# Kernel optimization log

Measured on AMD Instinct MI355X. Metric: run time of the kernel, lower is better.

Reference implementation:

```python
import jax, jax.numpy as jnp
import numpy as np

B, C, W, H = 4, 256, 64, 64

def setup_inputs() -> dict:
    key = jax.random.key(0)
    ks = jax.random.split(key, 6)
    return {
        "fm_source": jax.random.normal(ks[0], (B, C, W, H), dtype=jnp.float32),
        "fm_reference": jax.random.normal(ks[1], (B, C, W, H), dtype=jnp.float32),
        "w_lambda": jax.random.normal(ks[2], (1, C, 1, 1), dtype=jnp.float32) * 0.05,
        "b_lambda": jax.random.normal(ks[3], (1,), dtype=jnp.float32) * 0.05,
        "w_beta": jax.random.normal(ks[4], (1, C, 1, 1), dtype=jnp.float32) * 0.05,
        "b_beta": jax.random.normal(ks[5], (1,), dtype=jnp.float32) * 0.05,
    }

def reference(fm_source, fm_reference, w_lambda, b_lambda, w_beta, b_beta):
    b, c, w, h = fm_reference.shape
    n = w * h
    # 1x1 convs on the reference feature map -> per-pixel scalars, flattened to [B, N]
    wl = w_lambda.reshape(c)
    wb = w_beta.reshape(c)
    ref_flat = fm_reference.reshape(b, c, n)   # [B, C, N]
    src_flat = fm_source.reshape(b, c, n)      # [B, C, N]
    old_lambda = jnp.einsum("bcn,c->bn", ref_flat, wl) + b_lambda[0]  # [B, N]
    old_beta = jnp.einsum("bcn,c->bn", ref_flat, wb) + b_beta[0]      # [B, N]
    # energy[b, i, j] = <src pixel i, ref pixel j> over channels
    energy = jnp.einsum("bci,bcj->bij", src_flat, ref_flat)  # [B, N, N]
    attention = jax.nn.softmax(energy, axis=-1)              # softmax over ref pixels j
    # new_lambda[b, i] = sum_j old_lambda[b, j] * attention[b, i, j]
    new_lambda = jnp.einsum("bj,bij->bi", old_lambda, attention).reshape(b, 1, w, h)
    new_beta = jnp.einsum("bj,bij->bi", old_beta, attention).reshape(b, 1, w, h)
    # broadcast modulation over the 256 channels
    return new_lambda * fm_source + new_beta
```

## Files before the change

kernel.cpp:

```cpp
#include <hip/hip_runtime.h>


#define B_ 4
#define C_ 256
#define N_ 4096
#define LOG2E 1.44269504f
#define SHIFT2 86.5617f
#define JSLICE 8
#define BN_ (B_ * N_)
#define NT_ 16

typedef _Float16 half_t;
typedef _Float16 v8h  __attribute__((ext_vector_type(8)));
typedef float    v16f __attribute__((ext_vector_type(16)));

#define GLDS16(g, l) __builtin_amdgcn_global_load_lds(                         \
    (const __attribute__((address_space(1))) void*)(g),                        \
    (__attribute__((address_space(3))) void*)(l), 16, 0, 0)

#define TILE_SEC(T, ACC0, ACC1, LAM, BET, DO_FIN, FACC0, FACC1, FLAM, FBET)    \
  {                                                                            \
    __syncthreads();                                                           \
    if ((T) + 1 < NT_) {                                                       \
      const half_t* g = bBase + (size_t)((T) + 1) * 8192;                      \
      _Pragma("unroll")                                                        \
      for (int q = 0; q < 2; q++) {                                            \
        int chunk = q * 8 + wv;                                                \
        GLDS16(g + (size_t)chunk * 512 + (size_t)lane * 8,                     \
               &lds[((T) + 1) & 1][(size_t)chunk * 512]);                      \
      }                                                                        \
    }                                                                          \
    LAM = oL[(T) * 32 + l31];                                                  \
    BET = oB[(T) * 32 + l31];                                                  \
    const half_t* bt = lds[(T) & 1] + (size_t)lane * 8;                        \
    _Pragma("unroll")                                                          \
    for (int r = 0; r < 16; r++) { ACC0[r] = -SHIFT2; ACC1[r] = 0.f; }         \
    _Pragma("unroll")                                                          \
    for (int kb = 0; kb < 8; kb++) {                                           \
      ACC0 = __builtin_amdgcn_mfma_f32_32x32x16_f16(                           \
          a[kb], *(const v8h*)(bt + (size_t)kb * 512), ACC0, 0, 0, 0);         \
      ACC1 = __builtin_amdgcn_mfma_f32_32x32x16_f16(                           \
          a[kb + 8], *(const v8h*)(bt + (size_t)(kb + 8) * 512), ACC1, 0,0,0); \
      if (DO_FIN) {                                                            \
        _Pragma("unroll")                                                      \
        for (int rr = 2 * kb; rr < 2 * kb + 2; rr++) {                         \
          float p = __builtin_amdgcn_exp2f(FACC0[rr] + FACC1[rr]);             \
          sp[rr] += p; sl[rr] += p * FLAM; sb[rr] += p * FBET;                 \
        }                                                                      \
      }                                                                        \
    }                                                                          \
  }

__global__ void k_prep(const float* __restrict__ src,
                       const float* __restrict__ ref,
                       const float* __restrict__ wl,
                       const float* __restrict__ wb,
                       half_t* __restrict__ s16, half_t* __restrict__ r16,
                       float* __restrict__ oldLp, float* __restrict__ oldBp,
                       float* __restrict__ sums ) {
    __shared__ float tile[64][65];
    __shared__ float red[8][64];
    int z  = blockIdx.z;
    int isRef = z >> 2;
    int b  = z & 3;
    const float* in  = isRef ? ref : src;
    half_t*      out = isRef ? r16 : s16;
    float scale      = isRef ? 1.0f : LOG2E;
    int c0 = blockIdx.y * 64;
    int n0 = blockIdx.x * 64;
    int tid = threadIdx.x;
    if (z == 0) {
        int gid = (blockIdx.y * 64 + blockIdx.x) * 256 + tid;
        if (gid < 3 * BN_) sums[gid] = 0.f;
    }
    int tx = tid & 15, ty = tid >> 4;
#pragma unroll
    for (int q = 0; q < 4; q++) {
        int c = ty + q * 16;
        float4 v = *(const float4*)(in + ((size_t)b * C_ + c0 + c) * N_ + n0 + tx * 4);
        tile[c][tx * 4 + 0] = v.x;
        tile[c][tx * 4 + 1] = v.y;
        tile[c][tx * 4 + 2] = v.z;
        tile[c][tx * 4 + 3] = v.w;
    }
    __syncthreads();
    int r   = tid & 31;
    int lhi = (tid >> 5) & 1;
    int wv  = tid >> 6;
#pragma unroll
    for (int nt = 0; nt < 2; nt++) {
        int nl = nt * 32 + r;
        v8h o;
#pragma unroll
        for (int e = 0; e < 8; e++)
            o[e] = (half_t)(tile[wv * 16 + lhi * 8 + e][nl] * scale);
        size_t tj = (size_t)(n0 >> 5) + nt;
        size_t kb = (size_t)(c0 >> 4) + wv;
        *(v8h*)(out + ((((size_t)b * 128 + tj) * 16 + kb) * 64 + (tid & 63)) * 8) = o;
    }
    if (!isRef) return;
    int n  = tid & 63;
    int cq = tid >> 6;
    float aL = 0.f, aB = 0.f;
#pragma unroll
    for (int c = 0; c < 16; c++) {
        float v = tile[cq * 16 + c][n];
        aL += v * wl[c0 + cq * 16 + c];
        aB += v * wb[c0 + cq * 16 + c];
    }
    red[cq][n]     = aL;
    red[4 + cq][n] = aB;
    __syncthreads();
    size_t slot = ((size_t)blockIdx.y * B_ + b) * N_ + n0;
    if (tid < 64) {
        oldLp[slot + tid] = red[0][tid] + red[1][tid] + red[2][tid] + red[3][tid];
    } else if (tid < 128) {
        int u = tid - 64;
        oldBp[slot + u] = red[4][u] + red[5][u] + red[6][u] + red[7][u];
    }
}

__global__ __launch_bounds__(512, 2) void k_flash(
        const half_t* __restrict__ sT, const half_t* __restrict__ rT,
        const float* __restrict__ oldLp, const float* __restrict__ oldBp,
        const float* __restrict__ bl, const float* __restrict__ bb,
        float* __restrict__ sumP, float* __restrict__ sumL,
        float* __restrict__ sumB) {
    __shared__ half_t lds[2][8192];
    __shared__ float oL[512], oB[512];
    int bid    = blockIdx.x;
    int b      = bid & 3;
    int jslice = (bid >> 2) & (JSLICE - 1);
    int iblock = bid >> 5;
    int tid    = threadIdx.x;
    int wv     = tid >> 6;
    int lane   = tid & 63;
    int l31    = lane & 31, lhi = lane >> 5;
    int ti     = iblock * 8 + wv;
    int i0     = ti * 32;
    int j0     = jslice * (N_ / JSLICE);
    int tj0    = j0 >> 5;

    const half_t* aP = sT + (((size_t)b * 128 + ti) * 16) * 512 + (size_t)lane * 8;
    v8h a[16];
#pragma unroll
    for (int kb = 0; kb < 16; kb++) a[kb] = *(const v8h*)(aP + (size_t)kb * 512);

    {
        float accL = bl[0], accB = bb[0];
        size_t base = (size_t)b * N_ + j0 + tid;
#pragma unroll
        for (int g = 0; g < 4; g++) {
            accL += oldLp[(size_t)g * BN_ + base];
            accB += oldBp[(size_t)g * BN_ + base];
        }
        oL[tid] = accL;
        oB[tid] = accB;
    }

    const half_t* bBase = rT + (((size_t)b * 128 + tj0) * 16) * 512;

    float sp[16], sl[16], sb[16];
#pragma unroll
    for (int r = 0; r < 16; r++) { sp[r] = 0.f; sl[r] = 0.f; sb[r] = 0.f; }

#pragma unroll
    for (int q = 0; q < 2; q++) {
        int chunk = q * 8 + wv;
        GLDS16(bBase + (size_t)chunk * 512 + (size_t)lane * 8,
               &lds[0][(size_t)chunk * 512]);
    }

    v16f accA0, accA1, accB0, accB1;
    float lamA = 0.f, betA = 0.f, lamB = 0.f, betB = 0.f;

    TILE_SEC(0, accA0, accA1, lamA, betA, false, accB0, accB1, lamB, betB)
    for (int pt = 0; pt < 7; pt++) {
        int t1 = 2 * pt + 1, t2 = 2 * pt + 2;
        TILE_SEC(t1, accB0, accB1, lamB, betB, true, accA0, accA1, lamA, betA)
        TILE_SEC(t2, accA0, accA1, lamA, betA, true, accB0, accB1, lamB, betB)
    }
    TILE_SEC(15, accB0, accB1, lamB, betB, true, accA0, accA1, lamA, betA)
#pragma unroll
    for (int r = 0; r < 16; r++) {
        float p = __builtin_amdgcn_exp2f(accB0[r] + accB1[r]);
        sp[r] += p; sl[r] += p * lamB; sb[r] += p * betB;
    }

#pragma unroll
    for (int r = 0; r < 16; r++) {
        float tp = sp[r], tl = sl[r], tb = sb[r];
#pragma unroll
        for (int m = 1; m <= 16; m <<= 1) {
            tp += __shfl_xor(tp, m, 64);
            tl += __shfl_xor(tl, m, 64);
            tb += __shfl_xor(tb, m, 64);
        }
        if (l31 == 0) {
            int row = (r & 3) + 8 * (r >> 2) + 4 * lhi;
            size_t ig = (size_t)b * N_ + i0 + row;
            atomicAdd(&sumP[ig], tp);
            atomicAdd(&sumL[ig], tl);
            atomicAdd(&sumB[ig], tb);
        }
    }
}

__global__ void k_post(const float* __restrict__ src,
                       const float* __restrict__ sums,
                       float* __restrict__ out) {
    int b  = blockIdx.x;
    int n0 = blockIdx.y * 1024;
    int c0 = blockIdx.z * 4;
    int t  = threadIdx.x;
    size_t bn = (size_t)b * N_ + n0 + t * 4;
    float4 sp = *(const float4*)(sums + bn);
    float4 sl = *(const float4*)(sums + BN_ + bn);
    float4 sb = *(const float4*)(sums + 2 * BN_ + bn);
    float4 L, T;
    L.x = sl.x / sp.x; L.y = sl.y / sp.y; L.z = sl.z / sp.z; L.w = sl.w / sp.w;
    T.x = sb.x / sp.x; T.y = sb.y / sp.y; T.z = sb.z / sp.z; T.w = sb.w / sp.w;
    const float* sp0 = src + ((size_t)b * C_ + c0) * N_ + n0 + t * 4;
    float*       op0 = out + ((size_t)b * C_ + c0) * N_ + n0 + t * 4;
#pragma unroll
    for (int c = 0; c < 4; c++) {
        float4 v = *(const float4*)(sp0 + (size_t)c * N_);
        float4 o;
        o.x = L.x * v.x + T.x;
        o.y = L.y * v.y + T.y;
        o.z = L.z * v.z + T.z;
        o.w = L.w * v.w + T.w;
        *(float4*)(op0 + (size_t)c * N_) = o;
    }
}

extern "C" void kernel_launch(void* const* d_in, const int* in_sizes, int n_in,
                              void* d_out, int out_size, void* d_ws, size_t ws_size,
                              hipStream_t stream) {
    const float* src = (const float*)d_in[0];
    const float* ref = (const float*)d_in[1];
    const float* wl  = (const float*)d_in[2];
    const float* bl  = (const float*)d_in[3];
    const float* wb  = (const float*)d_in[4];
    const float* bb  = (const float*)d_in[5];
    float* out = (float*)d_out;

    float* oldLp = (float*)d_ws;
    float* oldBp = oldLp + 4 * BN_;
    float* sums  = oldBp + 4 * BN_;
    float* sumP  = sums;
    float* sumL  = sums + BN_;
    float* sumB  = sums + 2 * BN_;
    size_t needF  = (size_t)11 * BN_ * sizeof(float);
    size_t need16 = (size_t)2 * B_ * N_ * C_ * sizeof(half_t);
    half_t* s16;
    if (ws_size >= needF + need16) s16 = (half_t*)((char*)d_ws + needF);
    else                           s16 = (half_t*)d_out;
    half_t* r16 = s16 + (size_t)B_ * N_ * C_;

    k_prep<<<dim3(N_ / 64, C_ / 64, 8), 256, 0, stream>>>(
        src, ref, wl, wb, s16, r16, oldLp, oldBp, sums);
    k_flash<<<B_ * JSLICE * 16, 512, 0, stream>>>(
        s16, r16, oldLp, oldBp, bl, bb, sumP, sumL, sumB);
    k_post<<<dim3(B_, N_ / 1024, C_ / 4), 256, 0, stream>>>(src, sums, out);
}
```

Baseline: 148.1 us.

## Replace atomic reductions with per-slice partial buffers and add combine kernel

The flash kernel now writes per-j-slice partial sums of the exponentials, lambda-weighted and beta-weighted terms into separate buffers instead of atomically adding into shared accumulators. A new combine kernel sums the slices and computes the final divisions, which also removes the zeroing of the sum buffers from the prep kernel. A small new kernel pre-reduces the per-channel-group partial 1x1 conv outputs plus bias once, and the flash kernel reads lambda/beta straight from global memory instead of staging them in LDS. This removes atomic contention and redundant per-block reductions, at the cost of two extra kernel launches and more workspace traffic.

```diff
diff --git a/kernel.cpp b/kernel.cpp
--- a/kernel.cpp
+++ b/kernel.cpp
@@ -30,8 +30,8 @@
                &lds[((T) + 1) & 1][(size_t)chunk * 512]);                      \
       }                                                                        \
     }                                                                          \
-    LAM = oL[(T) * 32 + l31];                                                  \
-    BET = oB[(T) * 32 + l31];                                                  \
+    LAM = oLp[(T) * 32];                                                       \
+    BET = oBp[(T) * 32];                                                       \
     const half_t* bt = lds[(T) & 1] + (size_t)lane * 8;                        \
     _Pragma("unroll")                                                          \
     for (int r = 0; r < 16; r++) { ACC0[r] = -SHIFT2; ACC1[r] = 0.f; }         \
@@ -56,8 +56,7 @@
                        const float* __restrict__ wl,
                        const float* __restrict__ wb,
                        half_t* __restrict__ s16, half_t* __restrict__ r16,
-                       float* __restrict__ oldLp, float* __restrict__ oldBp,
-                       float* __restrict__ sums ) {
+                       float* __restrict__ oldLp, float* __restrict__ oldBp) {
     __shared__ float tile[64][65];
     __shared__ float red[8][64];
     int z  = blockIdx.z;
@@ -69,10 +68,6 @@
     int c0 = blockIdx.y * 64;
     int n0 = blockIdx.x * 64;
     int tid = threadIdx.x;
-    if (z == 0) {
-        int gid = (blockIdx.y * 64 + blockIdx.x) * 256 + tid;
-        if (gid < 3 * BN_) sums[gid] = 0.f;
-    }
     int tx = tid & 15, ty = tid >> 4;
 #pragma unroll
     for (int q = 0; q < 4; q++) {
@@ -120,14 +115,29 @@
     }
 }
 
+__global__ void k_fin(const float* __restrict__ oldLp,
+                      const float* __restrict__ oldBp,
+                      const float* __restrict__ bl, const float* __restrict__ bb,
+                      float* __restrict__ oldL, float* __restrict__ oldB) {
+    size_t g4 = ((size_t)blockIdx.x * 256 + threadIdx.x) * 4;
+    float4 aL = {bl[0], bl[0], bl[0], bl[0]};
+    float4 aB = {bb[0], bb[0], bb[0], bb[0]};
+#pragma unroll
+    for (int g = 0; g < 4; g++) {
+        float4 pL = *(const float4*)(oldLp + (size_t)g * BN_ + g4);
+        float4 pB = *(const float4*)(oldBp + (size_t)g * BN_ + g4);
+        aL.x += pL.x; aL.y += pL.y; aL.z += pL.z; aL.w += pL.w;
+        aB.x += pB.x; aB.y += pB.y; aB.z += pB.z; aB.w += pB.w;
+    }
+    *(float4*)(oldL + g4) = aL;
+    *(float4*)(oldB + g4) = aB;
+}
+
 __global__ __launch_bounds__(512, 2) void k_flash(
         const half_t* __restrict__ sT, const half_t* __restrict__ rT,
-        const float* __restrict__ oldLp, const float* __restrict__ oldBp,
-        const float* __restrict__ bl, const float* __restrict__ bb,
-        float* __restrict__ sumP, float* __restrict__ sumL,
-        float* __restrict__ sumB) {
+        const float* __restrict__ oldL, const float* __restrict__ oldB,
+        float* __restrict__ part ) {
     __shared__ half_t lds[2][8192];
-    __shared__ float oL[512], oB[512];
     int bid    = blockIdx.x;
     int b      = bid & 3;
     int jslice = (bid >> 2) & (JSLICE - 1);
@@ -146,19 +156,9 @@
 #pragma unroll
     for (int kb = 0; kb < 16; kb++) a[kb] = *(const v8h*)(aP + (size_t)kb * 512);
 
-    {
-        float accL = bl[0], accB = bb[0];
-        size_t base = (size_t)b * N_ + j0 + tid;
-#pragma unroll
-        for (int g = 0; g < 4; g++) {
-            accL += oldLp[(size_t)g * BN_ + base];
-            accB += oldBp[(size_t)g * BN_ + base];
-        }
-        oL[tid] = accL;
-        oB[tid] = accB;
-    }
-
     const half_t* bBase = rT + (((size_t)b * 128 + tj0) * 16) * 512;
+    const float*  oLp = oldL + (size_t)b * N_ + j0 + l31;
+    const float*  oBp = oldB + (size_t)b * N_ + j0 + l31;
 
     float sp[16], sl[16], sb[16];
 #pragma unroll
@@ -187,6 +187,9 @@
         sp[r] += p; sl[r] += p * lamB; sb[r] += p * betB;
     }
 
+    float* pSP = part + ((size_t)jslice * 3 + 0) * BN_;
+    float* pSL = part + ((size_t)jslice * 3 + 1) * BN_;
+    float* pSB = part + ((size_t)jslice * 3 + 2) * BN_;
 #pragma unroll
     for (int r = 0; r < 16; r++) {
         float tp = sp[r], tl = sl[r], tb = sb[r];
@@ -199,27 +202,35 @@
         if (l31 == 0) {
             int row = (r & 3) + 8 * (r >> 2) + 4 * lhi;
             size_t ig = (size_t)b * N_ + i0 + row;
-            atomicAdd(&sumP[ig], tp);
-            atomicAdd(&sumL[ig], tl);
-            atomicAdd(&sumB[ig], tb);
+            pSP[ig] = tp; pSL[ig] = tl; pSB[ig] = tb;
         }
     }
 }
 
+__global__ void k_comb(const float* __restrict__ part,
+                       float* __restrict__ newLT ) {
+    int g = blockIdx.x * 256 + threadIdx.x;
+    float sp = 0.f, sl = 0.f, sb = 0.f;
+#pragma unroll
+    for (int s = 0; s < JSLICE; s++) {
+        sp += part[((size_t)s * 3 + 0) * BN_ + g];
+        sl += part[((size_t)s * 3 + 1) * BN_ + g];
+        sb += part[((size_t)s * 3 + 2) * BN_ + g];
+    }
+    newLT[g]       = sl / sp;
+    newLT[BN_ + g] = sb / sp;
+}
+
 __global__ void k_post(const float* __restrict__ src,
-                       const float* __restrict__ sums,
+                       const float* __restrict__ newLT,
                        float* __restrict__ out) {
     int b  = blockIdx.x;
     int n0 = blockIdx.y * 1024;
     int c0 = blockIdx.z * 4;
     int t  = threadIdx.x;
     size_t bn = (size_t)b * N_ + n0 + t * 4;
-    float4 sp = *(const float4*)(sums + bn);
-    float4 sl = *(const float4*)(sums + BN_ + bn);
-    float4 sb = *(const float4*)(sums + 2 * BN_ + bn);
-    float4 L, T;
-    L.x = sl.x / sp.x; L.y = sl.y / sp.y; L.z = sl.z / sp.z; L.w = sl.w / sp.w;
-    T.x = sb.x / sp.x; T.y = sb.y / sp.y; T.z = sb.z / sp.z; T.w = sb.w / sp.w;
+    float4 L = *(const float4*)(newLT + bn);
+    float4 T = *(const float4*)(newLT + BN_ + bn);
     const float* sp0 = src + ((size_t)b * C_ + c0) * N_ + n0 + t * 4;
     float*       op0 = out + ((size_t)b * C_ + c0) * N_ + n0 + t * 4;
 #pragma unroll
@@ -245,13 +256,13 @@
     const float* bb  = (const float*)d_in[5];
     float* out = (float*)d_out;
 
-    float* oldLp = (float*)d_ws;
+    float* oldL  = (float*)d_ws;
+    float* oldB  = oldL + BN_;
+    float* oldLp = oldB + BN_;
     float* oldBp = oldLp + 4 * BN_;
-    float* sums  = oldBp + 4 * BN_;
-    float* sumP  = sums;
-    float* sumL  = sums + BN_;
-    float* sumB  = sums + 2 * BN_;
-    size_t needF  = (size_t)11 * BN_ * sizeof(float);
+    float* part  = oldBp + 4 * BN_;
+    float* newLT = part + (size_t)3 * JSLICE * BN_;
+    size_t needF  = ((size_t)2 + 8 + 3 * JSLICE + 2) * BN_ * sizeof(float);
     size_t need16 = (size_t)2 * B_ * N_ * C_ * sizeof(half_t);
     half_t* s16;
     if (ws_size >= needF + need16) s16 = (half_t*)((char*)d_ws + needF);
@@ -259,8 +270,9 @@
     half_t* r16 = s16 + (size_t)B_ * N_ * C_;
 
     k_prep<<<dim3(N_ / 64, C_ / 64, 8), 256, 0, stream>>>(
-        src, ref, wl, wb, s16, r16, oldLp, oldBp, sums);
-    k_flash<<<B_ * JSLICE * 16, 512, 0, stream>>>(
-        s16, r16, oldLp, oldBp, bl, bb, sumP, sumL, sumB);
-    k_post<<<dim3(B_, N_ / 1024, C_ / 4), 256, 0, stream>>>(src, sums, out);
-}
+        src, ref, wl, wb, s16, r16, oldLp, oldBp);
+    k_fin<<<BN_ / 1024, 256, 0, stream>>>(oldLp, oldBp, bl, bb, oldL, oldB);
+    k_flash<<<B_ * JSLICE * 16, 512, 0, stream>>>(s16, r16, oldL, oldB, part);
+    k_comb<<<BN_ / 256, 256, 0, stream>>>(part, newLT);
+    k_post<<<dim3(B_, N_ / 1024, C_ / 4), 256, 0, stream>>>(src, newLT, out);
+}
```

New measurement: 145.9 us. Within noise of the previous version (-1.5%).
